# Performance work log

Measured on AMD Instinct MI355X. Metric: run time of the kernel, lower is better.

The kernel has to match this reference:

```python
import jax, jax.numpy as jnp
import numpy as np

B, L, D, K = 8, 4096, 1024, 256

def setup_inputs() -> dict:
    key = jax.random.key(0)
    k1, k2, k3, k4 = jax.random.split(key, 4)
    x = jax.random.normal(k1, (B, L, D), dtype=jnp.float32)
    W_qkv = jax.random.normal(k2, (D, 3 * D), dtype=jnp.float32) * 0.02
    b_qkv = jnp.zeros((3 * D,), dtype=jnp.float32)
    H_k = jax.random.normal(k3, (L, K), dtype=jnp.float32)
    H_v = jax.random.normal(k4, (L, K), dtype=jnp.float32)
    return {"x": x, "W_qkv": W_qkv, "b_qkv": b_qkv, "H_k": H_k, "H_v": H_v}

def reference(x, W_qkv, b_qkv, H_k, H_v):
    Bn, Ln, Dn = x.shape
    qkv = x @ W_qkv + b_qkv                       # [B,L,3D]
    q, k, v = jnp.split(qkv, 3, axis=-1)          # each [B,L,D]
    K_proj = jnp.einsum('lk,bld->bkd', H_k, k)    # [B,K,D]
    V_proj = jnp.einsum('lk,bld->bkd', H_v, v)    # [B,K,D]
    scores = jnp.einsum('bld,bkd->blk', q, K_proj) / jnp.sqrt(jnp.asarray(Dn, x.dtype))
    weights = jax.nn.softmax(scores, axis=-1)     # [B,L,K]
    out = jnp.einsum('blk,bkd->bld', weights, V_proj)
    return out
```

## Files before the change

kernel.cpp:

```cpp
#include <hip/hip_runtime.h>


typedef __attribute__((ext_vector_type(8))) _Float16 half8;
typedef __attribute__((ext_vector_type(4))) _Float16 half4;
typedef __attribute__((ext_vector_type(4))) float f32x4;

#define AS1 __attribute__((address_space(1)))
#define AS3 __attribute__((address_space(3)))

__device__ __forceinline__ void gld_lds16(const void* g, void* l) {
    __builtin_amdgcn_global_load_lds((AS1 void*)g, (AS3 void*)l, 16, 0, 0);
}

template <typename T> struct is_f32 { static constexpr bool v = false; };
template <> struct is_f32<float> { static constexpr bool v = true; };

template <typename T> __device__ __forceinline__ T to_out(float v);
template <> __device__ __forceinline__ float    to_out<float>(float v) { return v; }
template <> __device__ __forceinline__ _Float16 to_out<_Float16>(float v) { return (_Float16)v; }

__device__ __forceinline__ half8 cvt_h8(f32x4 a, f32x4 b) {
    half8 h;
    h[0] = (_Float16)a[0]; h[1] = (_Float16)a[1]; h[2] = (_Float16)a[2]; h[3] = (_Float16)a[3];
    h[4] = (_Float16)b[0]; h[5] = (_Float16)b[1]; h[6] = (_Float16)b[2]; h[7] = (_Float16)b[3];
    return h;
}

template <typename OUT_T, bool SWIZ>
__global__ __launch_bounds__(256) void gemm_bt(
    const _Float16* __restrict__ A, long sA0, long sA1, long sA2, int lda,
    const _Float16* __restrict__ B, long sB0, long sB1, long sB2, int ldb,
    OUT_T* __restrict__ C, long sC0, long sC1, long sC2, int ldc,
    int nz0, int nz1, int NM, int NN, int Kd,
    const float* __restrict__ bias, long sb0,
    const float* __restrict__ rowv, const float* __restrict__ colv, float scale)
{
    {
        const int z = blockIdx.z;
        const int z0 = z % nz0, t = z / nz0, z1 = t % nz1, z2 = t / nz1;
        A += z0 * sA0 + z1 * sA1 + z2 * sA2;
        B += z0 * sB0 + z1 * sB1 + z2 * sB2;
        C += z0 * sC0 + z1 * sC1 + z2 * sC2;
        if (bias) bias += (long)z0 * sb0;
    }
    int mb, nb;
    if (SWIZ) {
        const int g = blockIdx.x, r = g % (8 * NN);
        mb = (g / (8 * NN)) * 8 + (r & 7);
        nb = r >> 3;
    } else {
        mb = blockIdx.x % NM;
        nb = blockIdx.x / NM;
    }
    const int tid = threadIdx.x, w = tid >> 6, ln = tid & 63;
    const int wm = (w >> 1) * 64, wn = (w & 1) * 64;

    __shared__ __attribute__((aligned(16))) _Float16 As[128 * 64];
    __shared__ __attribute__((aligned(16))) _Float16 Bs[128 * 64];

    f32x4 acc[4][4] = {};

    const int cb0 = w * 256;
    const _Float16* Ablk = A + (long)mb * 128 * lda;
    const _Float16* Bblk = B + (long)nb * 128 * ldb;

    const int lr = ln & 15, rs = ln & 7, kq = ln >> 4;

    for (int k0 = 0; k0 < Kd; k0 += 64) {
#pragma unroll
        for (int t = 0; t < 4; ++t) {
            const int ci = cb0 + t * 64 + ln;
            const int r = ci >> 3, kc = (ci & 7) ^ (r & 7);
            gld_lds16(Ablk + (long)r * lda + k0 + kc * 8, &As[(cb0 + t * 64) * 8]);
            gld_lds16(Bblk + (long)r * ldb + k0 + kc * 8, &Bs[(cb0 + t * 64) * 8]);
        }
        __syncthreads();
#pragma unroll
        for (int kh = 0; kh < 2; ++kh) {
            const int c = (((kh * 4) + kq) ^ rs) * 8;
            half8 af[4], bf[4];
#pragma unroll
            for (int i = 0; i < 4; ++i) {
                af[i] = *(const half8*)&As[(wm + i * 16 + lr) * 64 + c];
                bf[i] = *(const half8*)&Bs[(wn + i * 16 + lr) * 64 + c];
            }
#pragma unroll
            for (int i = 0; i < 4; ++i)
#pragma unroll
                for (int j = 0; j < 4; ++j)
                    acc[i][j] = __builtin_amdgcn_mfma_f32_16x16x32_f16(af[i], bf[j], acc[i][j], 0, 0, 0);
        }
        __syncthreads();
    }

    const int crow = mb * 128 + wm + (kq << 2);
    const int ccol = nb * 128 + wn + lr;
#pragma unroll
    for (int i = 0; i < 4; ++i)
#pragma unroll
        for (int r = 0; r < 4; ++r) {
            const long row = crow + i * 16 + r;
#pragma unroll
            for (int j = 0; j < 4; ++j) {
                const int col = ccol + j * 16;
                float v = acc[i][j][r] * scale;
                if (bias) v += bias[col];
                if (rowv) v += rowv[row] * colv[col];
                if constexpr (is_f32<OUT_T>::v)
                    __builtin_nontemporal_store(v, &C[row * ldc + col]);
                else
                    C[row * ldc + col] = to_out<OUT_T>(v);
            }
        }
}

__global__ __launch_bounds__(256) void score_softmax(
    const float* __restrict__ X, const _Float16* __restrict__ Bm,
    const float* __restrict__ cb, _Float16* __restrict__ Wts)
{
    const int b = blockIdx.z, mb = blockIdx.x;
    const float* Ab = X + (long)b * 4194304 + (long)mb * 131072;
    const _Float16* Bb = Bm + (long)b * 262144;
    const int tid = threadIdx.x, w = tid >> 6, ln = tid & 63;
    const int lr = ln & 15, rs = ln & 7, kq = ln >> 4;

    __shared__ __attribute__((aligned(16))) _Float16 SM[24576];
    _Float16* As = SM;
    _Float16* Bs = SM + 8192;

    f32x4 acc[2][16] = {};

    for (int k0 = 0; k0 < 1024; k0 += 64) {
        f32x4 pa[4][2];
#pragma unroll
        for (int t = 0; t < 4; ++t) {
            const int ci = w * 256 + t * 64 + ln;
            const int r = ci >> 3, kc = (ci & 7) ^ (r & 7);
            const float* ap = Ab + (long)r * 1024 + k0 + kc * 8;
            pa[t][0] = *(const f32x4*)ap;
            pa[t][1] = *(const f32x4*)(ap + 4);
        }
#pragma unroll
        for (int t = 0; t < 8; ++t) {
            const int cbase = w * 512 + t * 64;
            const int ci = cbase + ln, r = ci >> 3, kc = (ci & 7) ^ (r & 7);
            gld_lds16(Bb + (long)r * 1024 + k0 + kc * 8, &Bs[cbase * 8]);
        }
#pragma unroll
        for (int t = 0; t < 4; ++t) {
            const int ci = w * 256 + t * 64 + ln;
            *(half8*)&As[ci * 8] = cvt_h8(pa[t][0], pa[t][1]);
        }
        __syncthreads();
#pragma unroll
        for (int kh = 0; kh < 2; ++kh) {
            const int c = (((kh * 4) + kq) ^ rs) * 8;
            const half8 af0 = *(const half8*)&As[(w * 32 + lr) * 64 + c];
            const half8 af1 = *(const half8*)&As[(w * 32 + 16 + lr) * 64 + c];
#pragma unroll
            for (int j = 0; j < 16; ++j) {
                const half8 bf = *(const half8*)&Bs[(j * 16 + lr) * 64 + c];
                acc[0][j] = __builtin_amdgcn_mfma_f32_16x16x32_f16(af0, bf, acc[0][j], 0, 0, 0);
                acc[1][j] = __builtin_amdgcn_mfma_f32_16x16x32_f16(af1, bf, acc[1][j], 0, 0, 0);
            }
        }
        __syncthreads();
    }

    float cbl[16];
    const float* cbb = cb + b * 256;
#pragma unroll
    for (int j = 0; j < 16; ++j) cbl[j] = cbb[j * 16 + lr];

#pragma unroll
    for (int i = 0; i < 2; ++i)
#pragma unroll
        for (int r = 0; r < 4; ++r) {
            float m = -3.0e38f;
#pragma unroll
            for (int j = 0; j < 16; ++j) {
                float v = acc[i][j][r] + cbl[j];
                acc[i][j][r] = v;
                m = fmaxf(m, v);
            }
            m = fmaxf(m, __shfl_xor(m, 1, 64)); m = fmaxf(m, __shfl_xor(m, 2, 64));
            m = fmaxf(m, __shfl_xor(m, 4, 64)); m = fmaxf(m, __shfl_xor(m, 8, 64));
            float s = 0.f;
#pragma unroll
            for (int j = 0; j < 16; ++j) {
                float e = __expf(acc[i][j][r] - m);
                acc[i][j][r] = e;
                s += e;
            }
            s += __shfl_xor(s, 1, 64); s += __shfl_xor(s, 2, 64);
            s += __shfl_xor(s, 4, 64); s += __shfl_xor(s, 8, 64);
            const float inv = 1.0f / s;
#pragma unroll
            for (int j = 0; j < 16; ++j) acc[i][j][r] *= inv;
        }

#pragma unroll
    for (int i = 0; i < 2; ++i) {
        __syncthreads();
#pragma unroll
        for (int r = 0; r < 4; ++r)
#pragma unroll
            for (int j = 0; j < 16; ++j)
                SM[(w * 16 + kq * 4 + r) * 264 + j * 16 + lr] = (_Float16)acc[i][j][r];
        __syncthreads();
#pragma unroll
        for (int u = 0; u < 8; ++u) {
            const int idx = tid + 256 * u, row = idx >> 5, ci2 = idx & 31;
            const half8 v = *(const half8*)&SM[row * 264 + ci2 * 8];
            const long grow = (long)b * 4096 + mb * 128 + (row >> 4) * 32 + i * 16 + (row & 15);
            *(half8*)&Wts[grow * 256 + ci2 * 8] = v;
        }
    }
}

__global__ __launch_bounds__(256) void tr64(const float* __restrict__ src,
                                            _Float16* __restrict__ dst,
                                            _Float16* __restrict__ dsth,
                                            int R, int C, long sbatch, long dbatch) {
    __shared__ float T[64 * 65];
    const float* s = src + (long)blockIdx.z * sbatch;
    _Float16* d = dst + (long)blockIdx.z * dbatch;
    _Float16* dh = dsth ? dsth + (long)blockIdx.z * sbatch : nullptr;
    const int c0 = blockIdx.x * 64, r0 = blockIdx.y * 64;
    const int t = threadIdx.x;
    {
        const int row = t >> 2, cp = (t & 3) * 16;
        const float* sp = s + (long)(r0 + row) * C + c0 + cp;
        const float4 v0 = *(const float4*)(sp + 0);
        const float4 v1 = *(const float4*)(sp + 4);
        const float4 v2 = *(const float4*)(sp + 8);
        const float4 v3 = *(const float4*)(sp + 12);
        float* Tr = &T[row * 65 + cp];
        Tr[ 0] = v0.x; Tr[ 1] = v0.y; Tr[ 2] = v0.z; Tr[ 3] = v0.w;
        Tr[ 4] = v1.x; Tr[ 5] = v1.y; Tr[ 6] = v1.z; Tr[ 7] = v1.w;
        Tr[ 8] = v2.x; Tr[ 9] = v2.y; Tr[10] = v2.z; Tr[11] = v2.w;
        Tr[12] = v3.x; Tr[13] = v3.y; Tr[14] = v3.z; Tr[15] = v3.w;
        if (dh) {
            half8 h0, h1;
            h0[0] = (_Float16)v0.x; h0[1] = (_Float16)v0.y;
            h0[2] = (_Float16)v0.z; h0[3] = (_Float16)v0.w;
            h0[4] = (_Float16)v1.x; h0[5] = (_Float16)v1.y;
            h0[6] = (_Float16)v1.z; h0[7] = (_Float16)v1.w;
            h1[0] = (_Float16)v2.x; h1[1] = (_Float16)v2.y;
            h1[2] = (_Float16)v2.z; h1[3] = (_Float16)v2.w;
            h1[4] = (_Float16)v3.x; h1[5] = (_Float16)v3.y;
            h1[6] = (_Float16)v3.z; h1[7] = (_Float16)v3.w;
            _Float16* dp = dh + (long)(r0 + row) * C + c0 + cp;
            *(half8*)(dp + 0) = h0;
            *(half8*)(dp + 8) = h1;
        }
    }
    __syncthreads();
    {
        const int qq = t & 7, cc = t >> 3;
#pragma unroll
        for (int it = 0; it < 2; ++it) {
            const int col = cc + it * 32;
            half8 o;
#pragma unroll
            for (int u = 0; u < 8; ++u) o[u] = (_Float16)T[(qq * 8 + u) * 65 + col];
            *(half8*)(d + (long)(c0 + col) * R + r0 + qq * 8) = o;
        }
    }
}

__global__ void colsum2(const float* __restrict__ Hk, const float* __restrict__ Hv,
                        float* __restrict__ sk, float* __restrict__ sv) {
    const float* H = blockIdx.y ? Hv : Hk;
    float* s = blockIdx.y ? sv : sk;
    const int c = threadIdx.x;
    const long r0 = (long)blockIdx.x * 64;
    float acc = 0.f;
    for (int r = 0; r < 64; ++r) acc += H[(r0 + r) * 256 + c];
    atomicAdd(s + c, acc);
}

__global__ void bias_vecs(const float* __restrict__ W, const float* __restrict__ b,
                          float* __restrict__ gh) {
    const int wid = blockIdx.x * 4 + (threadIdx.x >> 6);
    const int ln = threadIdx.x & 63;
    float acc = 0.f;
    if (wid < 1024) {
        for (int j = 0; j < 16; ++j) { int d = ln + 64 * j; acc += b[d] * W[(long)wid * 3072 + 1024 + d]; }
    } else if (wid < 2048) {
        for (int j = 0; j < 16; ++j) { int d = ln + 64 * j; acc += b[1024 + d] * W[(long)(wid - 1024) * 3072 + d]; }
    } else if (wid == 2048) {
        for (int j = 0; j < 16; ++j) { int d = ln + 64 * j; acc += b[d] * b[1024 + d]; }
    } else return;
#pragma unroll
    for (int o = 32; o > 0; o >>= 1) acc += __shfl_xor(acc, o, 64);
    if (!ln) gh[wid] = acc * 0.03125f;
}

__global__ void cb_kernel(const _Float16* __restrict__ Pk, const float* __restrict__ gh,
                          const float* __restrict__ sk, float* __restrict__ cb) {
    const int wid = blockIdx.x * 4 + (threadIdx.x >> 6);
    const int ln = threadIdx.x & 63;
    const _Float16* row = Pk + (long)wid * 1024;
    float acc = 0.f;
    for (int j = 0; j < 16; ++j) { int c = ln + 64 * j; acc += (float)row[c] * gh[c]; }
#pragma unroll
    for (int o = 32; o > 0; o >>= 1) acc += __shfl_xor(acc, o, 64);
    if (!ln) cb[wid] = acc + sk[wid & 255] * gh[2048];
}

__global__ void reduce_kv(const float* __restrict__ P, _Float16* __restrict__ Pkv) {
    const long o = ((long)blockIdx.x * 256 + threadIdx.x) * 4;
    const int kv = (int)(o >> 21), b = (int)(o >> 18) & 7;
    const long r = o & 262143;
    const long i = (long)b * 524288 + (long)kv * 262144 + r;
    float4 a = *(const float4*)(P + i);
    float4 bb = *(const float4*)(P + i + 4194304);
    half4 out;
    out[0] = (_Float16)(a.x + bb.x); out[1] = (_Float16)(a.y + bb.y);
    out[2] = (_Float16)(a.z + bb.z); out[3] = (_Float16)(a.w + bb.w);
    *(half4*)(Pkv + o) = out;
}

extern "C" void kernel_launch(void* const* d_in, const int* in_sizes, int n_in,
                              void* d_out, int out_size, void* d_ws, size_t ws_size,
                              hipStream_t stream) {
    const float* x    = (const float*)d_in[0];
    const float* Wq   = (const float*)d_in[1];
    const float* bqkv = (const float*)d_in[2];
    const float* Hk   = (const float*)d_in[3];
    const float* Hv   = (const float*)d_in[4];
    float* out = (float*)d_out;

    char* p = (char*)d_ws;
    auto take = [&](size_t n) { char* r = p; p += (n + 255) & ~(size_t)255; return r; };
    _Float16* xt  = (_Float16*)take(33554432ull * 2);
    _Float16* Wt  = (_Float16*)take(3145728ull * 2);
    _Float16* Wh  = (_Float16*)take(3145728ull * 2);
    _Float16* Hkv = (_Float16*)take(2097152ull * 2);
    _Float16* Pkv = (_Float16*)take(4194304ull * 2);
    _Float16* VpT = (_Float16*)take(2097152ull * 2);
    _Float16* Gt  = (_Float16*)take(1048576ull * 2);
    _Float16* Mt  = (_Float16*)take(2097152ull * 2);
    float*    gh  = (float*)take(2049 * 4);
    float*    sk  = (float*)take(512 * 4);
    float*    sv  = sk + 256;
    float*    cbv = (float*)take(2048 * 4);
    float*    P32 = (float*)take(8388608ull * 4);
    _Float16* wts = (_Float16*)take(8388608ull * 2);

    const dim3 B256(256);

    tr64<<<dim3(16, 64, 8), B256, 0, stream>>>(x, xt, nullptr, 4096, 1024, 4194304, 4194304);
    tr64<<<dim3(48, 16, 1), B256, 0, stream>>>(Wq, Wt, Wh, 1024, 3072, 0, 0);
    tr64<<<dim3(4, 64, 1), B256, 0, stream>>>(Hk, Hkv, nullptr, 4096, 256, 0, 0);
    tr64<<<dim3(4, 64, 1), B256, 0, stream>>>(Hv, Hkv + 1048576, nullptr, 4096, 256, 0, 0);
    hipMemsetAsync(sk, 0, 512 * 4, stream);
    colsum2<<<dim3(64, 2, 1), B256, 0, stream>>>(Hk, Hv, sk, sv);
    bias_vecs<<<513, B256, 0, stream>>>(Wq, bqkv, gh);

    gemm_bt<_Float16, true><<<dim3(64, 1, 1), B256, 0, stream>>>(
        Wh, 0, 0, 0, 3072, Wh + 1024, 0, 0, 0, 3072, Gt, 0, 0, 0, 1024,
        1, 1, 8, 8, 1024, nullptr, 0, nullptr, nullptr, 1.0f);
    gemm_bt<float, false><<<dim3(32, 1, 16), B256, 0, stream>>>(
        Hkv, 0, 2048, 0, 4096, xt, 4194304, 2048, 0, 4096,
        P32, 524288, 4194304, 0, 1024,
        8, 2, 4, 8, 2048, nullptr, 0, nullptr, nullptr, 1.0f);
    reduce_kv<<<4096, B256, 0, stream>>>(P32, Pkv);
    gemm_bt<_Float16, true><<<dim3(16, 1, 8), B256, 0, stream>>>(
        Wt + 2097152, 0, 0, 0, 1024, Pkv + 2097152, 262144, 0, 0, 1024,
        VpT, 262144, 0, 0, 256,
        8, 1, 8, 2, 1024, nullptr, 0, bqkv + 2048, sv, 1.0f);
    gemm_bt<_Float16, false><<<dim3(16, 1, 8), B256, 0, stream>>>(
        Pkv, 262144, 0, 0, 1024, Gt, 0, 0, 0, 1024,
        Mt, 262144, 0, 0, 1024,
        8, 1, 2, 8, 1024, nullptr, 0, sk, gh + 1024, 0.03125f);
    cb_kernel<<<512, B256, 0, stream>>>(Pkv, gh, sk, cbv);
    score_softmax<<<dim3(32, 1, 8), B256, 0, stream>>>(x, Mt, cbv, wts);
    gemm_bt<float, true><<<dim3(256, 1, 8), B256, 0, stream>>>(
        wts, 1048576, 0, 0, 256, VpT, 262144, 0, 0, 256,
        out, 4194304, 0, 0, 1024,
        8, 1, 32, 8, 256, nullptr, 0, nullptr, nullptr, 1.0f);
}
```

Baseline: 492.5 us.

## Fuse transpose of x and H into a TN GEMM reading fp32 directly

Drops the separate transposes of x (32M elements) and H_k/H_v to fp16. A new GEMM kernel reads fp32 x and H along the sequence dimension, converts to fp16 in registers, and writes swizzled LDS tiles. Its output layout is changed to a batch-interleaved K/V layout, and downstream strides are updated to match. This removes a full round trip of x through memory, but the new kernel uses register-staged global loads rather than async LDS loads.

```diff
diff --git a/kernel.cpp b/kernel.cpp
--- a/kernel.cpp
+++ b/kernel.cpp
@@ -112,6 +112,97 @@
                     C[row * ldc + col] = to_out<OUT_T>(v);
             }
         }
+}
+
+__global__ __launch_bounds__(256) void gemm_tn_pkv(
+    const float* __restrict__ X, const float* __restrict__ Hk,
+    const float* __restrict__ Hv, float* __restrict__ P32)
+{
+    const int z = blockIdx.z, b = z & 7, ks = z >> 3;
+    const int mb = blockIdx.x & 7, nb = blockIdx.x >> 3;
+    const float* Ab = X + (long)b * 4194304 + (long)ks * 2097152 + mb * 128;
+    const float* Bb = (nb >= 2 ? Hv + (nb - 2) * 128 : Hk + nb * 128) + (long)ks * 524288;
+    float* Cb = P32 + (long)ks * 4194304 + (long)b * 524288;
+
+    const int tid = threadIdx.x, w = tid >> 6, ln = tid & 63;
+    const int wm = (w >> 1) * 64, wn = (w & 1) * 64;
+    const int lr = ln & 15, rs = ln & 7, kq = ln >> 4;
+    const int skq = (tid >> 2) & 7;
+    const int sm0 = ((tid & 3) | ((tid >> 5) << 2)) * 4;
+
+    __shared__ __attribute__((aligned(16))) _Float16 As[128 * 64];
+    __shared__ __attribute__((aligned(16))) _Float16 Bs[128 * 64];
+
+    f32x4 acc[4][4] = {};
+    f32x4 va[8], vb[8];
+
+#pragma unroll
+    for (int i = 0; i < 8; ++i)
+        va[i] = *(const f32x4*)(Ab + (long)(skq * 8 + i) * 1024 + sm0);
+#pragma unroll
+    for (int i = 0; i < 8; ++i)
+        vb[i] = *(const f32x4*)(Bb + (long)(skq * 8 + i) * 256 + sm0);
+
+    for (int k0 = 0; k0 < 2048; k0 += 64) {
+#pragma unroll
+        for (int j = 0; j < 4; ++j) {
+            half8 h;
+#pragma unroll
+            for (int i = 0; i < 8; ++i) h[i] = (_Float16)va[i][j];
+            *(half8*)&As[(sm0 + j) * 64 + ((skq ^ ((sm0 + j) & 7)) << 3)] = h;
+        }
+#pragma unroll
+        for (int j = 0; j < 4; ++j) {
+            half8 h;
+#pragma unroll
+            for (int i = 0; i < 8; ++i) h[i] = (_Float16)vb[i][j];
+            *(half8*)&Bs[(sm0 + j) * 64 + ((skq ^ ((sm0 + j) & 7)) << 3)] = h;
+        }
+        __syncthreads();
+        if (k0 + 64 < 2048) {
+            const long kn = k0 + 64;
+#pragma unroll
+            for (int i = 0; i < 8; ++i)
+                va[i] = *(const f32x4*)(Ab + (kn + skq * 8 + i) * 1024 + sm0);
+#pragma unroll
+            for (int i = 0; i < 8; ++i)
+                vb[i] = *(const f32x4*)(Bb + (kn + skq * 8 + i) * 256 + sm0);
+        }
+#pragma unroll
+        for (int kh = 0; kh < 2; ++kh) {
+            const int c = (((kh * 4) + kq) ^ rs) * 8;
+            half8 af[4], bf[4];
+#pragma unroll
+            for (int i = 0; i < 4; ++i) {
+                af[i] = *(const half8*)&As[(wm + i * 16 + lr) * 64 + c];
+                bf[i] = *(const half8*)&Bs[(wn + i * 16 + lr) * 64 + c];
+            }
+#pragma unroll
+            for (int i = 0; i < 4; ++i)
+#pragma unroll
+                for (int j = 0; j < 4; ++j)
+                    acc[i][j] = __builtin_amdgcn_mfma_f32_16x16x32_f16(af[i], bf[j], acc[i][j], 0, 0, 0);
+        }
+        __syncthreads();
+    }
+
+    const int crow = mb * 128 + wm + (kq << 2);
+    const int ccol = nb * 128 + wn + lr;
+#pragma unroll
+    for (int i = 0; i < 4; ++i)
+#pragma unroll
+        for (int j = 0; j < 4; ++j)
+            *(f32x4*)&Cb[(long)(ccol + j * 16) * 1024 + crow + i * 16] = acc[i][j];
+}
+
+__global__ void reduce_kv2(const float* __restrict__ P, _Float16* __restrict__ Pkv) {
+    const long o = ((long)blockIdx.x * 256 + threadIdx.x) * 4;
+    float4 a = *(const float4*)(P + o);
+    float4 bb = *(const float4*)(P + o + 4194304);
+    half4 out;
+    out[0] = (_Float16)(a.x + bb.x); out[1] = (_Float16)(a.y + bb.y);
+    out[2] = (_Float16)(a.z + bb.z); out[3] = (_Float16)(a.w + bb.w);
+    *(half4*)(Pkv + o) = out;
 }
 
 __global__ __launch_bounds__(256) void score_softmax(
@@ -301,25 +392,12 @@
                           const float* __restrict__ sk, float* __restrict__ cb) {
     const int wid = blockIdx.x * 4 + (threadIdx.x >> 6);
     const int ln = threadIdx.x & 63;
-    const _Float16* row = Pk + (long)wid * 1024;
+    const _Float16* row = Pk + (long)(wid >> 8) * 524288 + (long)(wid & 255) * 1024;
     float acc = 0.f;
     for (int j = 0; j < 16; ++j) { int c = ln + 64 * j; acc += (float)row[c] * gh[c]; }
 #pragma unroll
     for (int o = 32; o > 0; o >>= 1) acc += __shfl_xor(acc, o, 64);
     if (!ln) cb[wid] = acc + sk[wid & 255] * gh[2048];
-}
-
-__global__ void reduce_kv(const float* __restrict__ P, _Float16* __restrict__ Pkv) {
-    const long o = ((long)blockIdx.x * 256 + threadIdx.x) * 4;
-    const int kv = (int)(o >> 21), b = (int)(o >> 18) & 7;
-    const long r = o & 262143;
-    const long i = (long)b * 524288 + (long)kv * 262144 + r;
-    float4 a = *(const float4*)(P + i);
-    float4 bb = *(const float4*)(P + i + 4194304);
-    half4 out;
-    out[0] = (_Float16)(a.x + bb.x); out[1] = (_Float16)(a.y + bb.y);
-    out[2] = (_Float16)(a.z + bb.z); out[3] = (_Float16)(a.w + bb.w);
-    *(half4*)(Pkv + o) = out;
 }
 
 extern "C" void kernel_launch(void* const* d_in, const int* in_sizes, int n_in,
@@ -334,10 +412,8 @@
 
     char* p = (char*)d_ws;
     auto take = [&](size_t n) { char* r = p; p += (n + 255) & ~(size_t)255; return r; };
-    _Float16* xt  = (_Float16*)take(33554432ull * 2);
     _Float16* Wt  = (_Float16*)take(3145728ull * 2);
     _Float16* Wh  = (_Float16*)take(3145728ull * 2);
-    _Float16* Hkv = (_Float16*)take(2097152ull * 2);
     _Float16* Pkv = (_Float16*)take(4194304ull * 2);
     _Float16* VpT = (_Float16*)take(2097152ull * 2);
     _Float16* Gt  = (_Float16*)take(1048576ull * 2);
@@ -351,28 +427,23 @@
 
     const dim3 B256(256);
 
-    tr64<<<dim3(16, 64, 8), B256, 0, stream>>>(x, xt, nullptr, 4096, 1024, 4194304, 4194304);
     tr64<<<dim3(48, 16, 1), B256, 0, stream>>>(Wq, Wt, Wh, 1024, 3072, 0, 0);
-    tr64<<<dim3(4, 64, 1), B256, 0, stream>>>(Hk, Hkv, nullptr, 4096, 256, 0, 0);
-    tr64<<<dim3(4, 64, 1), B256, 0, stream>>>(Hv, Hkv + 1048576, nullptr, 4096, 256, 0, 0);
     hipMemsetAsync(sk, 0, 512 * 4, stream);
     colsum2<<<dim3(64, 2, 1), B256, 0, stream>>>(Hk, Hv, sk, sv);
     bias_vecs<<<513, B256, 0, stream>>>(Wq, bqkv, gh);
 
+    gemm_tn_pkv<<<dim3(32, 1, 16), B256, 0, stream>>>(x, Hk, Hv, P32);
+    reduce_kv2<<<4096, B256, 0, stream>>>(P32, Pkv);
+
     gemm_bt<_Float16, true><<<dim3(64, 1, 1), B256, 0, stream>>>(
         Wh, 0, 0, 0, 3072, Wh + 1024, 0, 0, 0, 3072, Gt, 0, 0, 0, 1024,
         1, 1, 8, 8, 1024, nullptr, 0, nullptr, nullptr, 1.0f);
-    gemm_bt<float, false><<<dim3(32, 1, 16), B256, 0, stream>>>(
-        Hkv, 0, 2048, 0, 4096, xt, 4194304, 2048, 0, 4096,
-        P32, 524288, 4194304, 0, 1024,
-        8, 2, 4, 8, 2048, nullptr, 0, nullptr, nullptr, 1.0f);
-    reduce_kv<<<4096, B256, 0, stream>>>(P32, Pkv);
     gemm_bt<_Float16, true><<<dim3(16, 1, 8), B256, 0, stream>>>(
-        Wt + 2097152, 0, 0, 0, 1024, Pkv + 2097152, 262144, 0, 0, 1024,
+        Wt + 2097152, 0, 0, 0, 1024, Pkv + 262144, 524288, 0, 0, 1024,
         VpT, 262144, 0, 0, 256,
         8, 1, 8, 2, 1024, nullptr, 0, bqkv + 2048, sv, 1.0f);
     gemm_bt<_Float16, false><<<dim3(16, 1, 8), B256, 0, stream>>>(
-        Pkv, 262144, 0, 0, 1024, Gt, 0, 0, 0, 1024,
+        Pkv, 524288, 0, 0, 1024, Gt, 0, 0, 0, 1024,
         Mt, 262144, 0, 0, 1024,
         8, 1, 2, 8, 1024, nullptr, 0, sk, gh + 1024, 0.03125f);
     cb_kernel<<<512, B256, 0, stream>>>(Pkv, gh, sk, cbv);
```

Measured after the change: 468.2 us. 1.05x faster.
